# Performance work log

Hardware: AMD Instinct MI355X
Metric: run time of the kernel (lower is better)

## Reference

```python
import jax, jax.numpy as jnp
import numpy as np

HIDDEN = 2048
EXPERTS = 8
INTER = 1024
TOP_K = 2
AUX_LOSS_WEIGHT = 0.01
TOKENS = 8192


def setup_inputs() -> dict:
    key = jax.random.key(0)
    k_x, k_g, k_w1, k_w2 = jax.random.split(key, 4)
    x = jax.random.normal(k_x, (TOKENS, HIDDEN), dtype=jnp.float32)
    # nn.Linear(hidden, experts, bias=False): weight is [E, H], applied as x @ W^T
    gate_w = jax.random.normal(k_g, (EXPERTS, HIDDEN), dtype=jnp.float32) * 0.02
    w1 = jax.random.normal(k_w1, (EXPERTS, HIDDEN, INTER), dtype=jnp.float32) * 0.02
    w2 = jax.random.normal(k_w2, (EXPERTS, INTER, HIDDEN), dtype=jnp.float32) * 0.02
    return {"x": x, "gate_w": gate_w, "w1": w1, "w2": w2}


def _moe_forward(x, gate_w, w1, w2):
    E = gate_w.shape[0]
    logits = x @ gate_w.T                              # [T, E]
    probs = jax.nn.softmax(logits, axis=-1)            # [T, E]
    topk_w, topk_idx = jax.lax.top_k(probs, TOP_K)     # [T, K]
    topk_w = topk_w / jnp.sum(topk_w, axis=-1, keepdims=True)

    # load-balancing aux loss: E * sum_e f_e * P_e
    one_hot = jax.nn.one_hot(topk_idx, E, dtype=probs.dtype)   # [T, K, E]
    f = jnp.mean(jnp.sum(one_hot, axis=1), axis=0)             # fraction of tokens per expert
    P = jnp.mean(probs, axis=0)                                # mean router prob per expert
    aux_loss = AUX_LOSS_WEIGHT * E * jnp.sum(f * P)

    # grouped expert MLP (dense-over-experts formulation, same math as
    # permute -> grouped GEMM -> unpermute):
    h = jnp.einsum('th,ehi->tei', x, w1)               # [T, E, I]
    h = jax.nn.gelu(h)
    y = jnp.einsum('tei,eih->teh', h, w2)              # [T, E, H]

    # combine: gather each token's top-k expert outputs and weight them
    y_sel = jnp.take_along_axis(y, topk_idx[:, :, None], axis=1)  # [T, K, H]
    out = jnp.sum(y_sel * topk_w[:, :, None], axis=1)             # [T, H]
    return out, aux_loss


def reference(x, gate_w, w1, w2):
    return _moe_forward(x, gate_w, w1, w2)
```

## Files before the change

kernel.cpp:

```cpp
#include <hip/hip_runtime.h>
#include <hip/hip_fp16.h>
#include <cmath>

#define T_TOKENS 8192
#define HID 2048
#define NEXP 8
#define INTERM 1024
#define GATE_NB 2048
#define MAX_TT 136
#define MAX_TT2 72
#define GEMM_NB 512
#define GEMM2_NB 256

typedef _Float16 f16x8 __attribute__((ext_vector_type(8)));
typedef _Float16 f16x4 __attribute__((ext_vector_type(4)));
typedef float f32x4 __attribute__((ext_vector_type(4)));

static __device__ __forceinline__ float gelu_tanh(float v) {
    return 0.5f * v * (1.0f + tanhf(0.79788456080286535588f * (v + 0.044715f * v * v * v)));
}

static __device__ __forceinline__ void glds16(const void* g, void* l) {
    __builtin_amdgcn_global_load_lds((const __attribute__((address_space(1))) void*)g,
                                     (__attribute__((address_space(3))) void*)l, 16, 0, 0);
}

static __device__ __forceinline__ f16x8 lds_read(const _Float16* base, int row, int chunk) {
    int phys = chunk ^ (row & 7);
    return *reinterpret_cast<const f16x8*>(
        reinterpret_cast<const char*>(base) + row * 128 + phys * 16);
}

static __device__ __forceinline__ void tconv_body(const float* __restrict__ in,
                                                  _Float16* __restrict__ out,
                                                  int R, int C, int bx, int by, int bz) {
    __shared__ float t[32][33];
    int r0 = by * 32, c0 = bx * 32;
    int tid = threadIdx.x;
    int r = tid >> 3, c4 = (tid & 7) * 4;
    const float4 v = *reinterpret_cast<const float4*>(&in[((size_t)bz * R + (r0 + r)) * C + c0 + c4]);
    t[r][c4 + 0] = v.x; t[r][c4 + 1] = v.y; t[r][c4 + 2] = v.z; t[r][c4 + 3] = v.w;
    __syncthreads();
    int oc = tid >> 3;
    int or4 = (tid & 7) * 4;
    f16x4 o;
    o[0] = (_Float16)t[or4 + 0][oc];
    o[1] = (_Float16)t[or4 + 1][oc];
    o[2] = (_Float16)t[or4 + 2][oc];
    o[3] = (_Float16)t[or4 + 3][oc];
    *reinterpret_cast<f16x4*>(&out[((size_t)bz * C + (c0 + oc)) * R + r0 + or4]) = o;
}

static __device__ __forceinline__ void gate_body(const float* __restrict__ x,
                                                 const float* __restrict__ gw,
                                                 _Float16* __restrict__ xh,
                                                 int* __restrict__ tk_idx, float* __restrict__ tk_w,
                                                 int* __restrict__ part_cnt,
                                                 double* __restrict__ part_sumP, int gid) {
    __shared__ double sds[4][NEXP];
    __shared__ int sci[4][NEXP];
    int w = threadIdx.x >> 6;
    int lane = threadIdx.x & 63;
    int t = gid * 4 + w;

    const float4* xr = (const float4*)(x + (size_t)t * HID);
    _Float16* xo = xh + (size_t)t * HID;
    double acc[NEXP];
#pragma unroll
    for (int e = 0; e < NEXP; e++) acc[e] = 0.0;
#pragma unroll
    for (int i = 0; i < HID / 256; i++) {
        float4 xv = xr[i * 64 + lane];
        f16x4 h;
        h[0] = (_Float16)xv.x; h[1] = (_Float16)xv.y;
        h[2] = (_Float16)xv.z; h[3] = (_Float16)xv.w;
        *reinterpret_cast<f16x4*>(xo + i * 256 + lane * 4) = h;
#pragma unroll
        for (int e = 0; e < NEXP; e++) {
            float4 gv = ((const float4*)(gw + (size_t)e * HID))[i * 64 + lane];
            acc[e] += (double)xv.x * (double)gv.x + (double)xv.y * (double)gv.y
                    + (double)xv.z * (double)gv.z + (double)xv.w * (double)gv.w;
        }
    }
#pragma unroll
    for (int e = 0; e < NEXP; e++) {
#pragma unroll
        for (int off = 32; off > 0; off >>= 1) acc[e] += __shfl_xor(acc[e], off, 64);
    }
    double mx = acc[0];
#pragma unroll
    for (int e = 1; e < NEXP; e++) mx = acc[e] > mx ? acc[e] : mx;
    double ex[NEXP];
    double sum = 0.0;
#pragma unroll
    for (int e = 0; e < NEXP; e++) { ex[e] = exp(acc[e] - mx); sum += ex[e]; }
    int i0 = 0;
#pragma unroll
    for (int e = 1; e < NEXP; e++) if (ex[e] > ex[i0]) i0 = e;
    int i1 = (i0 == 0) ? 1 : 0;
#pragma unroll
    for (int e = 0; e < NEXP; e++) if (e != i0 && ex[e] > ex[i1]) i1 = e;
    double p0 = ex[i0], p1 = ex[i1];
    double t2 = p0 + p1;
    if (lane == 0) {
        tk_idx[2 * t] = i0; tk_idx[2 * t + 1] = i1;
        tk_w[2 * t] = (float)(p0 / t2); tk_w[2 * t + 1] = (float)(p1 / t2);
#pragma unroll
        for (int e = 0; e < NEXP; e++) {
            sds[w][e] = ex[e] / sum;
            sci[w][e] = (e == i0 ? 1 : 0) + (e == i1 ? 1 : 0);
        }
    }
    __syncthreads();
    if (threadIdx.x < NEXP) {
        int e = threadIdx.x;
        part_sumP[e * GATE_NB + gid] = sds[0][e] + sds[1][e] + sds[2][e] + sds[3][e];
        part_cnt[e * GATE_NB + gid]  = sci[0][e] + sci[1][e] + sci[2][e] + sci[3][e];
    }
}

__global__ __launch_bounds__(256) void prep_kernel(const float* __restrict__ x,
                                                   const float* __restrict__ gw,
                                                   const float* __restrict__ w1,
                                                   const float* __restrict__ w2,
                                                   _Float16* __restrict__ xh,
                                                   _Float16* __restrict__ w1t,
                                                   _Float16* __restrict__ w2t,
                                                   int* __restrict__ tk_idx, float* __restrict__ tk_w,
                                                   int* __restrict__ part_cnt,
                                                   double* __restrict__ part_sumP) {
    int bid = blockIdx.x;
    if (bid < 16384) {
        int bx = bid & 31, by = (bid >> 5) & 63, bz = bid >> 11;
        tconv_body(w1, w1t, HID, INTERM, bx, by, bz);
    } else if (bid < 32768) {
        int r = bid - 16384;
        int bx = r & 63, by = (r >> 6) & 31, bz = r >> 11;
        tconv_body(w2, w2t, INTERM, HID, bx, by, bz);
    } else {
        gate_body(x, gw, xh, tk_idx, tk_w, part_cnt, part_sumP, bid - 32768);
    }
}

__global__ __launch_bounds__(256) void finalize_kernel(const int* __restrict__ part_cnt,
                                                       const double* __restrict__ part_sumP,
                                                       int* __restrict__ cnt, int* __restrict__ offs,
                                                       int* __restrict__ cursor,
                                                       int* __restrict__ ttab,
                                                       int* __restrict__ ttab2,
                                                       int* __restrict__ nmt,
                                                       int* __restrict__ steal,
                                                       float* __restrict__ aux_out) {
    __shared__ double swv[4];
    __shared__ int cwv[4];
    __shared__ double sE[NEXP];
    __shared__ int cE[NEXP];
    int w = threadIdx.x >> 6;
    int lane = threadIdx.x & 63;
    for (int e = 0; e < NEXP; e++) {
        double s = 0.0; int c = 0;
        for (int j = threadIdx.x; j < GATE_NB; j += 256) {
            s += part_sumP[e * GATE_NB + j];
            c += part_cnt[e * GATE_NB + j];
        }
#pragma unroll
        for (int off = 32; off > 0; off >>= 1) {
            s += __shfl_xor(s, off, 64);
            c += __shfl_xor(c, off, 64);
        }
        if (lane == 0) { swv[w] = s; cwv[w] = c; }
        __syncthreads();
        if (threadIdx.x == 0) {
            sE[e] = swv[0] + swv[1] + swv[2] + swv[3];
            cE[e] = cwv[0] + cwv[1] + cwv[2] + cwv[3];
        }
        __syncthreads();
    }
    if (threadIdx.x == 0) {
        int off = 0;
        double aux = 0.0;
        int idx = 0, idx2 = 0;
#pragma unroll
        for (int e = 0; e < NEXP; e++) {
            cnt[e] = cE[e];
            offs[e] = off;
            off += cE[e];
            cursor[e] = 0;
            aux += ((double)cE[e] / (double)T_TOKENS) * (sE[e] / (double)T_TOKENS);
            int mt = (cE[e] + 127) >> 7;
            for (int m = 0; m < mt; m++) ttab[idx++] = (e << 16) | m;
            int mt2 = (cE[e] + 255) >> 8;
            for (int m = 0; m < mt2; m++) ttab2[idx2++] = (e << 16) | m;
        }
        nmt[0] = idx;
        nmt[1] = idx2;
        for (; idx < MAX_TT; idx++) ttab[idx] = -1;
        for (; idx2 < MAX_TT2; idx2++) ttab2[idx2] = -1;
        for (int i = 0; i < 16; i++) steal[i] = 0;
        aux_out[0] = (float)(0.01 * (double)NEXP * aux);
    }
}

__global__ void scatter_kernel(const int* __restrict__ tk_idx, const float* __restrict__ tk_w,
                               const int* __restrict__ offs, int* __restrict__ cursor,
                               int* __restrict__ row_tok, float* __restrict__ row_w,
                               int* __restrict__ tok_row) {
    int t = blockIdx.x * blockDim.x + threadIdx.x;
    int lane = threadIdx.x & 63;
    unsigned long long below = (lane == 0) ? 0ull : ((~0ull) >> (64 - lane));
    for (int k = 0; k < 2; k++) {
        int e = tk_idx[2 * t + k];
        float wv = tk_w[2 * t + k];
        int pos = 0;
#pragma unroll
        for (int ee = 0; ee < NEXP; ee++) {
            unsigned long long m = __ballot(e == ee);
            if (e == ee) {
                int rank = (int)__popcll(m & below);
                int leader = (int)__ffsll((unsigned long long)m) - 1;
                int b = 0;
                if (lane == leader) b = atomicAdd(&cursor[ee], (int)__popcll(m));
                b = __shfl(b, leader, 64);
                pos = b + rank;
            }
        }
        int r = offs[e] + pos;
        row_tok[r] = t;
        row_w[r] = wv;
        tok_row[2 * t + k] = r;
    }
}

template<bool GATHER, bool GELU, int KTOT, int NX>
__global__ __launch_bounds__(256, 2) void gemm8_kernel(
    const _Float16* __restrict__ Aglob,
    const _Float16* __restrict__ Bglob,
    const int* __restrict__ cnt, const int* __restrict__ offs,
    const int* __restrict__ row_tok,
    const int* __restrict__ ttab,
    const int* __restrict__ nmt,
    int* __restrict__ steal,
    _Float16* __restrict__ Out, int Ncols)
{
    constexpr int NT = KTOT / 64;
    __shared__ __align__(16) _Float16 As[2][128][64];
    __shared__ __align__(16) _Float16 Bs[2][128][64];
    __shared__ int s_it;

    int tid = threadIdx.x;
    int w = tid >> 6, lane = tid & 63;
    int wr = w >> 1, wc = w & 1;
    int fr = lane & 15, fq = lane >> 4;

    int n_items = nmt[0] * NX;
    int chunk = (n_items + 7) >> 3;
    int xcd = blockIdx.x & 7;

    int srow = tid >> 3;
    int lc = (tid & 7) ^ (srow & 7);

    _Float16* ldsA = &As[0][0][0] + w * 512;
    _Float16* ldsB = &Bs[0][0][0] + w * 512;

    for (;;) {
        __syncthreads();
        if (tid == 0) s_it = atomicAdd(&steal[xcd], 1);
        __syncthreads();
        int i = s_it;
        if (i >= chunk) break;
        int it = xcd * chunk + i;
        if (it >= n_items) break;

        int ent = ttab[it / NX];
        int e = ent >> 16;
        int m0 = (ent & 0xffff) << 7;
        int Ne = cnt[e];
        int base = offs[e];
        int n0 = (it & (NX - 1)) << 7;

        const _Float16* aS[4];
#pragma unroll
        for (int r = 0; r < 4; r++) {
            int ar = m0 + r * 32 + srow; if (ar >= Ne) ar = Ne - 1;
            int id = GATHER ? row_tok[base + ar] : (base + ar);
            aS[r] = Aglob + (size_t)id * KTOT + lc * 8;
        }
        const size_t bexp = (size_t)e * Ncols * KTOT;
        const _Float16* bS[4];
#pragma unroll
        for (int r = 0; r < 4; r++)
            bS[r] = Bglob + bexp + (size_t)(n0 + r * 32 + srow) * KTOT + lc * 8;

#define STAGE(S, KOFF) do {                                         \
        glds16(aS[0] + (KOFF), ldsA + (S) * 8192 + 0 * 2048);       \
        glds16(aS[1] + (KOFF), ldsA + (S) * 8192 + 1 * 2048);       \
        glds16(aS[2] + (KOFF), ldsA + (S) * 8192 + 2 * 2048);       \
        glds16(aS[3] + (KOFF), ldsA + (S) * 8192 + 3 * 2048);       \
        glds16(bS[0] + (KOFF), ldsB + (S) * 8192 + 0 * 2048);       \
        glds16(bS[1] + (KOFF), ldsB + (S) * 8192 + 1 * 2048);       \
        glds16(bS[2] + (KOFF), ldsB + (S) * 8192 + 2 * 2048);       \
        glds16(bS[3] + (KOFF), ldsB + (S) * 8192 + 3 * 2048);       \
    } while (0)

        f32x4 acc[4][4] = {};
        STAGE(0, 0);

        for (int j = 0; j < NT; ++j) {
            int slot = j & 1;
            const _Float16* Ab = &As[slot][0][0];
            const _Float16* Bb = &Bs[slot][0][0];
            if (j + 1 < NT) {
                STAGE(slot ^ 1, (j + 1) * 64);
                asm volatile("s_waitcnt vmcnt(8)" ::: "memory");
            } else {
                asm volatile("s_waitcnt vmcnt(0)" ::: "memory");
            }
            __builtin_amdgcn_s_barrier();

            f16x8 b_[4][2];
            {
                f16x8 a_[2][2];
#pragma unroll
                for (int i2 = 0; i2 < 2; i2++)
#pragma unroll
                    for (int k = 0; k < 2; k++)
                        a_[i2][k] = lds_read(Ab, wr * 64 + i2 * 16 + fr, k * 4 + fq);
#pragma unroll
                for (int jj = 0; jj < 4; jj++)
#pragma unroll
                    for (int k = 0; k < 2; k++)
                        b_[jj][k] = lds_read(Bb, wc * 64 + jj * 16 + fr, k * 4 + fq);
                asm volatile("s_waitcnt lgkmcnt(0)" ::: "memory");
                __builtin_amdgcn_s_setprio(1);
#pragma unroll
                for (int i2 = 0; i2 < 2; i2++)
#pragma unroll
                    for (int jj = 0; jj < 4; jj++)
#pragma unroll
                        for (int k = 0; k < 2; k++)
                            acc[i2][jj] = __builtin_amdgcn_mfma_f32_16x16x32_f16(
                                a_[i2][k], b_[jj][k], acc[i2][jj], 0, 0, 0);
                __builtin_amdgcn_s_setprio(0);
            }
            {
                f16x8 a_[2][2];
#pragma unroll
                for (int i2 = 0; i2 < 2; i2++)
#pragma unroll
                    for (int k = 0; k < 2; k++)
                        a_[i2][k] = lds_read(Ab, wr * 64 + (2 + i2) * 16 + fr, k * 4 + fq);
                asm volatile("s_waitcnt lgkmcnt(0)" ::: "memory");
                __builtin_amdgcn_s_setprio(1);
#pragma unroll
                for (int i2 = 0; i2 < 2; i2++)
#pragma unroll
                    for (int jj = 0; jj < 4; jj++)
#pragma unroll
                        for (int k = 0; k < 2; k++)
                            acc[2 + i2][jj] = __builtin_amdgcn_mfma_f32_16x16x32_f16(
                                a_[i2][k], b_[jj][k], acc[2 + i2][jj], 0, 0, 0);
                __builtin_amdgcn_s_setprio(0);
            }
            __builtin_amdgcn_s_barrier();
        }
#undef STAGE

#pragma unroll
        for (int mi = 0; mi < 4; mi++) {
#pragma unroll
            for (int r = 0; r < 4; r++) {
                int row = m0 + wr * 64 + mi * 16 + fq * 4 + r;
                if (row < Ne) {
                    _Float16* dst = Out + (size_t)(base + row) * Ncols + n0 + wc * 64 + fr;
#pragma unroll
                    for (int ni = 0; ni < 4; ni++) {
                        float v = acc[mi][ni][r];
                        if (GELU) v = gelu_tanh(v);
                        dst[ni * 16] = (_Float16)v;
                    }
                }
            }
        }
    }
}

template<int KTOT, int NX>
__global__ __launch_bounds__(512, 2) void gemm256_kernel(
    const _Float16* __restrict__ Aglob,
    const _Float16* __restrict__ Bglob,
    const int* __restrict__ cnt, const int* __restrict__ offs,
    const int* __restrict__ ttab2,
    const int* __restrict__ nmt,
    int* __restrict__ steal,
    _Float16* __restrict__ Out, int Ncols)
{
    constexpr int NT = KTOT / 64;
    __shared__ __align__(16) _Float16 As[2][256][64];
    __shared__ __align__(16) _Float16 Bs[2][256][64];
    __shared__ int s_it;

    int tid = threadIdx.x;
    int w = tid >> 6, lane = tid & 63;
    int wr = w >> 2, wc = w & 3;
    int fr = lane & 15, fq = lane >> 4;

    int n_items = nmt[1] * NX;
    int chunk = (n_items + 7) >> 3;
    int xcd = blockIdx.x & 7;

    int grow = lane >> 3;
    int lc = (lane & 7) ^ grow;

    _Float16* ldsA = &As[0][0][0] + (w * 32) * 64;
    _Float16* ldsB = &Bs[0][0][0] + (w * 32) * 64;

    for (;;) {
        __syncthreads();
        if (tid == 0) s_it = atomicAdd(&steal[xcd], 1);
        __syncthreads();
        int i = s_it;
        if (i >= chunk) break;
        int it = xcd * chunk + i;
        if (it >= n_items) break;

        int ent = ttab2[it / NX];
        int e = ent >> 16;
        int m0 = (ent & 0xffff) << 8;
        int Ne = cnt[e];
        int base = offs[e];
        int n0 = (it & (NX - 1)) << 8;

        const _Float16* aS[4];
#pragma unroll
        for (int g = 0; g < 4; g++) {
            int ar = m0 + w * 32 + g * 8 + grow; if (ar >= Ne) ar = Ne - 1;
            aS[g] = Aglob + (size_t)(base + ar) * KTOT + lc * 8;
        }
        const size_t bexp = (size_t)e * Ncols * KTOT;
        const _Float16* bS[4];
#pragma unroll
        for (int g = 0; g < 4; g++)
            bS[g] = Bglob + bexp + (size_t)(n0 + w * 32 + g * 8 + grow) * KTOT + lc * 8;

        f32x4 acc[8][4] = {};

#pragma unroll
        for (int g = 0; g < 4; g++) glds16(aS[g], ldsA + g * 512);
#pragma unroll
        for (int g = 0; g < 4; g++) glds16(bS[g], ldsB + g * 512);

        for (int j = 0; j < NT; ++j) {
            int slot = j & 1;
            const _Float16* Ab = &As[slot][0][0];
            const _Float16* Bb = &Bs[slot][0][0];
            _Float16* An = ldsA + (slot ^ 1) * 16384;
            _Float16* Bn = ldsB + (slot ^ 1) * 16384;
            int koff = (j + 1) * 64;
            bool more = (j + 1 < NT);
            if (more) {
                glds16(aS[0] + koff, An + 0 * 512);
                glds16(aS[1] + koff, An + 1 * 512);
                asm volatile("s_waitcnt vmcnt(2)" ::: "memory");
            } else {
                asm volatile("s_waitcnt vmcnt(0)" ::: "memory");
            }
            __builtin_amdgcn_s_barrier();

            f16x8 b_[4];
            {
                f16x8 a_[4];
#pragma unroll
                for (int i2 = 0; i2 < 4; i2++)
                    a_[i2] = lds_read(Ab, wr * 128 + i2 * 16 + fr, fq);
#pragma unroll
                for (int jj = 0; jj < 4; jj++)
                    b_[jj] = lds_read(Bb, wc * 64 + jj * 16 + fr, fq);
                if (more) { glds16(aS[2] + koff, An + 2 * 512); glds16(aS[3] + koff, An + 3 * 512); }
                __builtin_amdgcn_s_barrier();
                asm volatile("s_waitcnt lgkmcnt(0)" ::: "memory");
                __builtin_amdgcn_s_setprio(1);
#pragma unroll
                for (int i2 = 0; i2 < 4; i2++)
#pragma unroll
                    for (int jj = 0; jj < 4; jj++)
                        acc[i2][jj] = __builtin_amdgcn_mfma_f32_16x16x32_f16(
                            a_[i2], b_[jj], acc[i2][jj], 0, 0, 0);
                __builtin_amdgcn_s_setprio(0);
                __builtin_amdgcn_s_barrier();
            }
            {
                f16x8 a_[4];
#pragma unroll
                for (int i2 = 0; i2 < 4; i2++)
                    a_[i2] = lds_read(Ab, wr * 128 + (4 + i2) * 16 + fr, fq);
                if (more) { glds16(bS[0] + koff, Bn + 0 * 512); glds16(bS[1] + koff, Bn + 1 * 512); }
                __builtin_amdgcn_s_barrier();
                asm volatile("s_waitcnt lgkmcnt(0)" ::: "memory");
                __builtin_amdgcn_s_setprio(1);
#pragma unroll
                for (int i2 = 0; i2 < 4; i2++)
#pragma unroll
                    for (int jj = 0; jj < 4; jj++)
                        acc[4 + i2][jj] = __builtin_amdgcn_mfma_f32_16x16x32_f16(
                            a_[i2], b_[jj], acc[4 + i2][jj], 0, 0, 0);
                __builtin_amdgcn_s_setprio(0);
                __builtin_amdgcn_s_barrier();
            }
            {
                f16x8 a_[4];
#pragma unroll
                for (int i2 = 0; i2 < 4; i2++)
                    a_[i2] = lds_read(Ab, wr * 128 + i2 * 16 + fr, 4 + fq);
#pragma unroll
                for (int jj = 0; jj < 4; jj++)
                    b_[jj] = lds_read(Bb, wc * 64 + jj * 16 + fr, 4 + fq);
                if (more) { glds16(bS[2] + koff, Bn + 2 * 512); glds16(bS[3] + koff, Bn + 3 * 512); }
                __builtin_amdgcn_s_barrier();
                asm volatile("s_waitcnt lgkmcnt(0)" ::: "memory");
                __builtin_amdgcn_s_setprio(1);
#pragma unroll
                for (int i2 = 0; i2 < 4; i2++)
#pragma unroll
                    for (int jj = 0; jj < 4; jj++)
                        acc[i2][jj] = __builtin_amdgcn_mfma_f32_16x16x32_f16(
                            a_[i2], b_[jj], acc[i2][jj], 0, 0, 0);
                __builtin_amdgcn_s_setprio(0);
                __builtin_amdgcn_s_barrier();
            }
            {
                f16x8 a_[4];
#pragma unroll
                for (int i2 = 0; i2 < 4; i2++)
                    a_[i2] = lds_read(Ab, wr * 128 + (4 + i2) * 16 + fr, 4 + fq);
                __builtin_amdgcn_s_barrier();
                asm volatile("s_waitcnt lgkmcnt(0)" ::: "memory");
                __builtin_amdgcn_s_setprio(1);
#pragma unroll
                for (int i2 = 0; i2 < 4; i2++)
#pragma unroll
                    for (int jj = 0; jj < 4; jj++)
                        acc[4 + i2][jj] = __builtin_amdgcn_mfma_f32_16x16x32_f16(
                            a_[i2], b_[jj], acc[4 + i2][jj], 0, 0, 0);
                __builtin_amdgcn_s_setprio(0);
                __builtin_amdgcn_s_barrier();
            }
        }

#pragma unroll
        for (int mi = 0; mi < 8; mi++) {
#pragma unroll
            for (int r = 0; r < 4; r++) {
                int row = m0 + wr * 128 + mi * 16 + fq * 4 + r;
                if (row < Ne) {
                    _Float16* dst = Out + (size_t)(base + row) * Ncols + n0 + wc * 64 + fr;
#pragma unroll
                    for (int ni = 0; ni < 4; ni++)
                        dst[ni * 16] = (_Float16)acc[mi][ni][r];
                }
            }
        }
    }
}

__global__ __launch_bounds__(256) void combine_kernel(const _Float16* __restrict__ y,
                                                      const int* __restrict__ tok_row,
                                                      const float* __restrict__ tk_w,
                                                      float* __restrict__ out) {
    int t = blockIdx.x;
    int c = threadIdx.x;
    int r0 = tok_row[2 * t], r1 = tok_row[2 * t + 1];
    float w0 = tk_w[2 * t], w1 = tk_w[2 * t + 1];
    f16x8 a = reinterpret_cast<const f16x8*>(y + (size_t)r0 * HID)[c];
    f16x8 b = reinterpret_cast<const f16x8*>(y + (size_t)r1 * HID)[c];
    float4 o0, o1;
    o0.x = w0 * (float)a[0] + w1 * (float)b[0];
    o0.y = w0 * (float)a[1] + w1 * (float)b[1];
    o0.z = w0 * (float)a[2] + w1 * (float)b[2];
    o0.w = w0 * (float)a[3] + w1 * (float)b[3];
    o1.x = w0 * (float)a[4] + w1 * (float)b[4];
    o1.y = w0 * (float)a[5] + w1 * (float)b[5];
    o1.z = w0 * (float)a[6] + w1 * (float)b[6];
    o1.w = w0 * (float)a[7] + w1 * (float)b[7];
    float4* dst = reinterpret_cast<float4*>(out + (size_t)t * HID + c * 8);
    dst[0] = o0;
    dst[1] = o1;
}

extern "C" void kernel_launch(void* const* d_in, const int* in_sizes, int n_in,
                              void* d_out, int out_size, void* d_ws, size_t ws_size,
                              hipStream_t stream) {
    const float* x  = (const float*)d_in[0];
    const float* gw = (const float*)d_in[1];
    const float* w1 = (const float*)d_in[2];
    const float* w2 = (const float*)d_in[3];
    float* out = (float*)d_out;
    char* ws = (char*)d_ws;

    int*    cnt       = (int*)(ws + 0);
    int*    cursor    = (int*)(ws + 64);
    int*    offs      = (int*)(ws + 128);
    int*    nmt       = (int*)(ws + 256);
    int*    steal     = (int*)(ws + 320);
    int*    ttab      = (int*)(ws + 512);
    int*    ttab2     = (int*)(ws + 2048);
    int*    part_cnt  = (int*)(ws + 4096);
    double* part_sumP = (double*)(ws + 131072);
    int*    row_tok   = (int*)(ws + 262144);
    float*  row_w     = (float*)(ws + 327680);
    int*    tk_idx    = (int*)(ws + 393216);
    float*  tk_w      = (float*)(ws + 458752);
    int*    tok_row   = (int*)(ws + 524288);
    const size_t OFF = 589824;
    _Float16* xh  = (_Float16*)(ws + OFF);
    _Float16* w1t = (_Float16*)(ws + OFF + (1ull << 25));
    _Float16* w2t = (_Float16*)(ws + OFF + (2ull << 25));
    _Float16* hh  = (_Float16*)(ws + OFF + (3ull << 25));
    _Float16* y   = (_Float16*)(ws + OFF);

    prep_kernel<<<32768 + GATE_NB, 256, 0, stream>>>(x, gw, w1, w2, xh, w1t, w2t,
                                                     tk_idx, tk_w, part_cnt, part_sumP);
    finalize_kernel<<<1, 256, 0, stream>>>(part_cnt, part_sumP, cnt, offs, cursor,
                                           ttab, ttab2, nmt, steal,
                                           out + (size_t)T_TOKENS * HID);
    scatter_kernel<<<T_TOKENS / 256, 256, 0, stream>>>(tk_idx, tk_w, offs, cursor,
                                                       row_tok, row_w, tok_row);

    gemm8_kernel<true, true, HID, INTERM / 128>
        <<<GEMM_NB, 256, 0, stream>>>(xh, w1t, cnt, offs, row_tok, ttab, nmt, steal, hh, INTERM);
    gemm256_kernel<INTERM, HID / 256>
        <<<GEMM2_NB, 512, 0, stream>>>(hh, w2t, cnt, offs, ttab2, nmt, steal + 8, y, HID);

    combine_kernel<<<T_TOKENS, 256, 0, stream>>>(y, tok_row, tk_w, out);
}
```

Measured before the change: 390.2 us.

## Halve GEMM1 K-tile to 32 and raise occupancy to four blocks per CU

The first expert GEMM now stages 32-wide K slices instead of 64, halving LDS use per block. It switches to a new XOR swizzle for the 64-byte rows, launch bounds of 4 blocks per CU, and twice as many persistent blocks. Each wave loads its own 32-row slab, and the setprio and two-phase MFMA split is replaced by a single 4x4 MFMA loop per step. The goal is more latency hiding through occupancy, at the cost of twice as many barriers and K iterations and tighter register limits.

```diff
diff --git a/kernel.cpp b/kernel.cpp
--- a/kernel.cpp
+++ b/kernel.cpp
@@ -9,7 +9,7 @@
 #define GATE_NB 2048
 #define MAX_TT 136
 #define MAX_TT2 72
-#define GEMM_NB 512
+#define GEMM1_NB 1024
 #define GEMM2_NB 256
 
 typedef _Float16 f16x8 __attribute__((ext_vector_type(8)));
@@ -29,6 +29,12 @@
     int phys = chunk ^ (row & 7);
     return *reinterpret_cast<const f16x8*>(
         reinterpret_cast<const char*>(base) + row * 128 + phys * 16);
+}
+
+static __device__ __forceinline__ f16x8 lds_read32(const _Float16* base, int row, int chunk) {
+    int phys = chunk ^ ((row >> 1) & 3);
+    return *reinterpret_cast<const f16x8*>(
+        reinterpret_cast<const char*>(base) + row * 64 + phys * 16);
 }
 
 static __device__ __forceinline__ void tconv_body(const float* __restrict__ in,
@@ -232,7 +238,7 @@
 }
 
 template<bool GATHER, bool GELU, int KTOT, int NX>
-__global__ __launch_bounds__(256, 2) void gemm8_kernel(
+__global__ __launch_bounds__(256, 4) void gemmf_kernel(
     const _Float16* __restrict__ Aglob,
     const _Float16* __restrict__ Bglob,
     const int* __restrict__ cnt, const int* __restrict__ offs,
@@ -242,9 +248,9 @@
     int* __restrict__ steal,
     _Float16* __restrict__ Out, int Ncols)
 {
-    constexpr int NT = KTOT / 64;
-    __shared__ __align__(16) _Float16 As[2][128][64];
-    __shared__ __align__(16) _Float16 Bs[2][128][64];
+    constexpr int NT = KTOT / 32;
+    __shared__ __align__(16) _Float16 As[2][128][32];
+    __shared__ __align__(16) _Float16 Bs[2][128][32];
     __shared__ int s_it;
 
     int tid = threadIdx.x;
@@ -256,11 +262,11 @@
     int chunk = (n_items + 7) >> 3;
     int xcd = blockIdx.x & 7;
 
-    int srow = tid >> 3;
-    int lc = (tid & 7) ^ (srow & 7);
-
-    _Float16* ldsA = &As[0][0][0] + w * 512;
-    _Float16* ldsB = &Bs[0][0][0] + w * 512;
+    int srow = lane >> 2;
+    int lc = (lane & 3) ^ ((lane >> 3) & 3);
+
+    _Float16* ldsA = &As[0][0][0] + w * 1024;
+    _Float16* ldsB = &Bs[0][0][0] + w * 1024;
 
     for (;;) {
         __syncthreads();
@@ -278,92 +284,58 @@
         int base = offs[e];
         int n0 = (it & (NX - 1)) << 7;
 
-        const _Float16* aS[4];
-#pragma unroll
-        for (int r = 0; r < 4; r++) {
-            int ar = m0 + r * 32 + srow; if (ar >= Ne) ar = Ne - 1;
+        const _Float16* aS[2];
+#pragma unroll
+        for (int g = 0; g < 2; g++) {
+            int ar = m0 + w * 32 + g * 16 + srow; if (ar >= Ne) ar = Ne - 1;
             int id = GATHER ? row_tok[base + ar] : (base + ar);
-            aS[r] = Aglob + (size_t)id * KTOT + lc * 8;
+            aS[g] = Aglob + (size_t)id * KTOT + lc * 8;
         }
         const size_t bexp = (size_t)e * Ncols * KTOT;
-        const _Float16* bS[4];
-#pragma unroll
-        for (int r = 0; r < 4; r++)
-            bS[r] = Bglob + bexp + (size_t)(n0 + r * 32 + srow) * KTOT + lc * 8;
-
-#define STAGE(S, KOFF) do {                                         \
-        glds16(aS[0] + (KOFF), ldsA + (S) * 8192 + 0 * 2048);       \
-        glds16(aS[1] + (KOFF), ldsA + (S) * 8192 + 1 * 2048);       \
-        glds16(aS[2] + (KOFF), ldsA + (S) * 8192 + 2 * 2048);       \
-        glds16(aS[3] + (KOFF), ldsA + (S) * 8192 + 3 * 2048);       \
-        glds16(bS[0] + (KOFF), ldsB + (S) * 8192 + 0 * 2048);       \
-        glds16(bS[1] + (KOFF), ldsB + (S) * 8192 + 1 * 2048);       \
-        glds16(bS[2] + (KOFF), ldsB + (S) * 8192 + 2 * 2048);       \
-        glds16(bS[3] + (KOFF), ldsB + (S) * 8192 + 3 * 2048);       \
+        const _Float16* bS[2];
+#pragma unroll
+        for (int g = 0; g < 2; g++)
+            bS[g] = Bglob + bexp + (size_t)(n0 + w * 32 + g * 16 + srow) * KTOT + lc * 8;
+
+#define STAGE1(S, KOFF) do {                                        \
+        glds16(aS[0] + (KOFF), ldsA + (S) * 4096 + 0 * 512);        \
+        glds16(aS[1] + (KOFF), ldsA + (S) * 4096 + 1 * 512);        \
+        glds16(bS[0] + (KOFF), ldsB + (S) * 4096 + 0 * 512);        \
+        glds16(bS[1] + (KOFF), ldsB + (S) * 4096 + 1 * 512);        \
     } while (0)
 
         f32x4 acc[4][4] = {};
-        STAGE(0, 0);
+        STAGE1(0, 0);
 
         for (int j = 0; j < NT; ++j) {
             int slot = j & 1;
             const _Float16* Ab = &As[slot][0][0];
             const _Float16* Bb = &Bs[slot][0][0];
             if (j + 1 < NT) {
-                STAGE(slot ^ 1, (j + 1) * 64);
-                asm volatile("s_waitcnt vmcnt(8)" ::: "memory");
+                STAGE1(slot ^ 1, (j + 1) * 32);
+                asm volatile("s_waitcnt vmcnt(4)" ::: "memory");
             } else {
                 asm volatile("s_waitcnt vmcnt(0)" ::: "memory");
             }
             __builtin_amdgcn_s_barrier();
 
-            f16x8 b_[4][2];
-            {
-                f16x8 a_[2][2];
-#pragma unroll
-                for (int i2 = 0; i2 < 2; i2++)
-#pragma unroll
-                    for (int k = 0; k < 2; k++)
-                        a_[i2][k] = lds_read(Ab, wr * 64 + i2 * 16 + fr, k * 4 + fq);
+            f16x8 a_[4], b_[4];
+#pragma unroll
+            for (int ii = 0; ii < 4; ii++)
+                a_[ii] = lds_read32(Ab, wr * 64 + ii * 16 + fr, fq);
+#pragma unroll
+            for (int jj = 0; jj < 4; jj++)
+                b_[jj] = lds_read32(Bb, wc * 64 + jj * 16 + fr, fq);
+#pragma unroll
+            for (int ii = 0; ii < 4; ii++)
 #pragma unroll
                 for (int jj = 0; jj < 4; jj++)
-#pragma unroll
-                    for (int k = 0; k < 2; k++)
-                        b_[jj][k] = lds_read(Bb, wc * 64 + jj * 16 + fr, k * 4 + fq);
-                asm volatile("s_waitcnt lgkmcnt(0)" ::: "memory");
-                __builtin_amdgcn_s_setprio(1);
-#pragma unroll
-                for (int i2 = 0; i2 < 2; i2++)
-#pragma unroll
-                    for (int jj = 0; jj < 4; jj++)
-#pragma unroll
-                        for (int k = 0; k < 2; k++)
-                            acc[i2][jj] = __builtin_amdgcn_mfma_f32_16x16x32_f16(
-                                a_[i2][k], b_[jj][k], acc[i2][jj], 0, 0, 0);
-                __builtin_amdgcn_s_setprio(0);
-            }
-            {
-                f16x8 a_[2][2];
-#pragma unroll
-                for (int i2 = 0; i2 < 2; i2++)
-#pragma unroll
-                    for (int k = 0; k < 2; k++)
-                        a_[i2][k] = lds_read(Ab, wr * 64 + (2 + i2) * 16 + fr, k * 4 + fq);
-                asm volatile("s_waitcnt lgkmcnt(0)" ::: "memory");
-                __builtin_amdgcn_s_setprio(1);
-#pragma unroll
-                for (int i2 = 0; i2 < 2; i2++)
-#pragma unroll
-                    for (int jj = 0; jj < 4; jj++)
-#pragma unroll
-                        for (int k = 0; k < 2; k++)
-                            acc[2 + i2][jj] = __builtin_amdgcn_mfma_f32_16x16x32_f16(
-                                a_[i2][k], b_[jj][k], acc[2 + i2][jj], 0, 0, 0);
-                __builtin_amdgcn_s_setprio(0);
-            }
+                    acc[ii][jj] = __builtin_amdgcn_mfma_f32_16x16x32_f16(
+                        a_[ii], b_[jj], acc[ii][jj], 0, 0, 0);
+            asm volatile("s_waitcnt lgkmcnt(0)" ::: "memory");
             __builtin_amdgcn_s_barrier();
         }
-#undef STAGE
+#undef STAGE1
 
 #pragma unroll
         for (int mi = 0; mi < 4; mi++) {
@@ -625,8 +597,8 @@
     scatter_kernel<<<T_TOKENS / 256, 256, 0, stream>>>(tk_idx, tk_w, offs, cursor,
                                                        row_tok, row_w, tok_row);
 
-    gemm8_kernel<true, true, HID, INTERM / 128>
-        <<<GEMM_NB, 256, 0, stream>>>(xh, w1t, cnt, offs, row_tok, ttab, nmt, steal, hh, INTERM);
+    gemmf_kernel<true, true, HID, INTERM / 128>
+        <<<GEMM1_NB, 256, 0, stream>>>(xh, w1t, cnt, offs, row_tok, ttab, nmt, steal, hh, INTERM);
     gemm256_kernel<INTERM, HID / 256>
         <<<GEMM2_NB, 512, 0, stream>>>(hh, w2t, cnt, offs, ttab2, nmt, steal + 8, y, HID);
 
```

Result: no change. 390.3 us (+0.0%).
